# Performance work log

Hardware: AMD Instinct MI355X
Metric: run time of the kernel (lower is better)

## Reference

```python
import jax, jax.numpy as jnp
import numpy as np
import math

N, N0, M, K, CIN, COUT, DIM = 50000, 50000, 32, 15, 64, 64, 3
POINT_INFLUENCE = 0.05
KERNEL_RADIUS = 1.5 * POINT_INFLUENCE  # _INFLUENCE_TO_RADIUS * point_influence


def setup_inputs() -> dict:
    key = jax.random.key(0)
    k1, k2, k3, k4, k5, k6 = jax.random.split(key, 6)
    query_points = jax.random.uniform(k1, (N, DIM), dtype=jnp.float32)
    support_points = jax.random.uniform(k2, (N0, DIM), dtype=jnp.float32)
    # index N0 is the shadow-neighbor index (padding for ragged neighborhoods)
    neighbors = jax.random.randint(k3, (N, M), 0, N0 + 1)
    x = jax.random.normal(k4, (N0, CIN), dtype=jnp.float32)
    # kernel point dispositions inside the kernel ball, center point at origin (fixed='center')
    kp = jax.random.normal(k5, (K, DIM), dtype=jnp.float32)
    kp = kp / jnp.linalg.norm(kp, axis=1, keepdims=True) * (KERNEL_RADIUS * 0.66)
    K_points = kp.at[0].set(0.0)
    # xavier_normal_ init for weight [K, CIN, COUT]
    std = math.sqrt(2.0 / (CIN + COUT))
    weight = jax.random.normal(k6, (K, CIN, COUT), dtype=jnp.float32) * std
    return dict(query_points=query_points, support_points=support_points,
                neighbors=neighbors, x=x, K_points=K_points, weight=weight)


def reference(query_points, support_points, neighbors, x, K_points, weight):
    # shadow point far away + zero shadow feature (handles padded neighbor index N0)
    shadow_pt = jnp.full((1, support_points.shape[1]), 1e6, support_points.dtype)
    sp = jnp.concatenate([support_points, shadow_pt], axis=0)          # [N0+1, 3]
    feats = jnp.concatenate([x, jnp.zeros((1, x.shape[1]), x.dtype)], axis=0)  # [N0+1, CIN]

    # gather & center neighborhoods: [N, M, 3]
    nb_pts = sp[neighbors] - query_points[:, None, :]

    # squared distance to each kernel point without materializing [N,M,K,3]:
    # ||n - k||^2 = ||n||^2 - 2 n.k + ||k||^2  -> [N, M, K]
    sq = (jnp.sum(nb_pts * nb_pts, axis=-1)[:, :, None]
          - 2.0 * jnp.einsum('nmd,kd->nmk', nb_pts, K_points)
          + jnp.sum(K_points * K_points, axis=-1))
    sq = jnp.maximum(sq, 0.0)

    # linear KP influence: clamp(1 - dist / point_influence, min=0) -> transpose to [N, K, M]
    all_weights = jnp.maximum(1.0 - jnp.sqrt(sq) / POINT_INFLUENCE, 0.0)
    all_weights = jnp.swapaxes(all_weights, 1, 2)                      # [N, K, M]

    nb_feats = feats[neighbors]                                        # [N, M, CIN]
    weighted = jnp.matmul(all_weights, nb_feats)                       # [N, K, CIN]
    # sum over kernel points of per-kernel-point matmuls ('sum' aggregation)
    out = jnp.einsum('nkc,kco->no', weighted, weight)                  # [N, COUT]
    return out
```

## Files before the change

kernel.cpp:

```cpp
#include <hip/hip_runtime.h>

#define N_Q   50000
#define N_S   50000
#define M_NB  32
#define K_PTS 15
#define CIN   64
#define COUT  64

__global__ __launch_bounds__(256) void kpconv_fused(
    const float* __restrict__ query,
    const float* __restrict__ support,
    const int*   __restrict__ neighbors,
    const float* __restrict__ x,
    const float* __restrict__ kpts,
    const float* __restrict__ weight,
    float*       __restrict__ out)
{
    __shared__ float s_kx[K_PTS], s_ky[K_PTS], s_kz[K_PTS], s_kk[K_PTS];
    __shared__ float s_bc[4][CIN];

    const int tid = threadIdx.x;
    if (tid < K_PTS) {
        float kx = kpts[tid * 3 + 0];
        float ky = kpts[tid * 3 + 1];
        float kz = kpts[tid * 3 + 2];
        s_kx[tid] = kx; s_ky[tid] = ky; s_kz[tid] = kz;
        s_kk[tid] = kx * kx + ky * ky + kz * kz;
    }
    __syncthreads();

    const int wv   = tid >> 6;
    const int lane = tid & 63;
    const int n    = blockIdx.x * 4 + wv;

    const int m   = lane & 31;
    const int idx = neighbors[n * M_NB + m];

    float dx = 0.f, dy = 0.f, dz = 0.f, nn = 1e30f;
    if (lane < 32 && idx < N_S) {
        const float qx = query[n * 3 + 0];
        const float qy = query[n * 3 + 1];
        const float qz = query[n * 3 + 2];
        dx = support[idx * 3 + 0] - qx;
        dy = support[idx * 3 + 1] - qy;
        dz = support[idx * 3 + 2] - qz;
        nn = dx * dx + dy * dy + dz * dz;
    }

    float tout = 0.f;

    if (__ballot(nn < 0.0101f)) {
        for (int k = 0; k < K_PTS; ++k) {
            float w = 0.f;
            if (nn < 0.0101f) {
                float dot = dx * s_kx[k] + dy * s_ky[k] + dz * s_kz[k];
                float sq  = fmaxf(nn - 2.f * dot + s_kk[k], 0.f);
                if (sq < 0.0025f)
                    w = 1.f - sqrtf(sq) * 20.f;
            }
            unsigned long long em = __ballot(w > 0.f);
            if (!em) continue;

            float racc = 0.f;
            do {
                const int   src  = __ffsll(em) - 1; em &= em - 1;
                const float wsrc = __shfl(w,   src);
                const int   isrc = __shfl(idx, src);
                racc = fmaf(wsrc, x[(size_t)isrc * CIN + lane], racc);
            } while (em);

            s_bc[wv][lane] = racc;
            asm volatile("" ::: "memory");
            const float* wk = weight + (size_t)k * CIN * COUT;
            float p0 = 0.f, p1 = 0.f, p2 = 0.f, p3 = 0.f;
            #pragma unroll 8
            for (int c = 0; c < CIN; c += 4) {
                p0 = fmaf(s_bc[wv][c + 0], wk[(c + 0) * COUT + lane], p0);
                p1 = fmaf(s_bc[wv][c + 1], wk[(c + 1) * COUT + lane], p1);
                p2 = fmaf(s_bc[wv][c + 2], wk[(c + 2) * COUT + lane], p2);
                p3 = fmaf(s_bc[wv][c + 3], wk[(c + 3) * COUT + lane], p3);
            }
            tout += (p0 + p1) + (p2 + p3);
        }
    }

    out[(size_t)n * COUT + lane] = tout;
}

extern "C" void kernel_launch(void* const* d_in, const int* in_sizes, int n_in,
                              void* d_out, int out_size, void* d_ws, size_t ws_size,
                              hipStream_t stream) {
    const float* query     = (const float*)d_in[0];
    const float* support   = (const float*)d_in[1];
    const int*   neighbors = (const int*)  d_in[2];
    const float* x         = (const float*)d_in[3];
    const float* kpts      = (const float*)d_in[4];
    const float* weight    = (const float*)d_in[5];
    float*       out       = (float*)d_out;

    kpconv_fused<<<N_Q / 4, 256, 0, stream>>>(
        query, support, neighbors, x, kpts, weight, out);
}
```

Baseline: 32.52 us.

## Pack two queries per wavefront using both 32-lane halves for neighbor geometry

Each 64-lane wavefront now handles two query points, with each half computing the neighbor distances for one query, and the block shrinks to 128 threads. The kernel-point weighting and feature accumulation loop over each half's active-neighbor mask in turn. The aim is to stop leaving half the lanes idle during the geometry phase and to halve the wavefront count. In exchange, the feature gather and weight matmul are serialized per query within a wave, and the inner code is duplicated.

```diff
diff --git a/kernel.cpp b/kernel.cpp
--- a/kernel.cpp
+++ b/kernel.cpp
@@ -7,7 +7,7 @@
 #define CIN   64
 #define COUT  64
 
-__global__ __launch_bounds__(256) void kpconv_fused(
+__global__ __launch_bounds__(128) void kpconv_fused2(
     const float* __restrict__ query,
     const float* __restrict__ support,
     const int*   __restrict__ neighbors,
@@ -17,7 +17,7 @@
     float*       __restrict__ out)
 {
     __shared__ float s_kx[K_PTS], s_ky[K_PTS], s_kz[K_PTS], s_kk[K_PTS];
-    __shared__ float s_bc[4][CIN];
+    __shared__ float s_bc[2][CIN];
 
     const int tid = threadIdx.x;
     if (tid < K_PTS) {
@@ -31,23 +31,22 @@
 
     const int wv   = tid >> 6;
     const int lane = tid & 63;
-    const int n    = blockIdx.x * 4 + wv;
+    const int base = blockIdx.x * 4 + wv * 2;
+    const int h    = lane >> 5;
+    const int n    = base + h;
+    const int m    = lane & 31;
 
-    const int m   = lane & 31;
     const int idx = neighbors[n * M_NB + m];
 
     float dx = 0.f, dy = 0.f, dz = 0.f, nn = 1e30f;
-    if (lane < 32 && idx < N_S) {
-        const float qx = query[n * 3 + 0];
-        const float qy = query[n * 3 + 1];
-        const float qz = query[n * 3 + 2];
-        dx = support[idx * 3 + 0] - qx;
-        dy = support[idx * 3 + 1] - qy;
-        dz = support[idx * 3 + 2] - qz;
+    if (idx < N_S) {
+        dx = support[idx * 3 + 0] - query[n * 3 + 0];
+        dy = support[idx * 3 + 1] - query[n * 3 + 1];
+        dz = support[idx * 3 + 2] - query[n * 3 + 2];
         nn = dx * dx + dy * dy + dz * dz;
     }
 
-    float tout = 0.f;
+    float toutA = 0.f, toutB = 0.f;
 
     if (__ballot(nn < 0.0101f)) {
         for (int k = 0; k < K_PTS; ++k) {
@@ -58,33 +57,61 @@
                 if (sq < 0.0025f)
                     w = 1.f - sqrtf(sq) * 20.f;
             }
-            unsigned long long em = __ballot(w > 0.f);
+            const unsigned long long em = __ballot(w > 0.f);
             if (!em) continue;
 
-            float racc = 0.f;
-            do {
-                const int   src  = __ffsll(em) - 1; em &= em - 1;
-                const float wsrc = __shfl(w,   src);
-                const int   isrc = __shfl(idx, src);
-                racc = fmaf(wsrc, x[(size_t)isrc * CIN + lane], racc);
-            } while (em);
+            const float* wk = weight + (size_t)k * CIN * COUT;
 
-            s_bc[wv][lane] = racc;
-            asm volatile("" ::: "memory");
-            const float* wk = weight + (size_t)k * CIN * COUT;
-            float p0 = 0.f, p1 = 0.f, p2 = 0.f, p3 = 0.f;
-            #pragma unroll 8
-            for (int c = 0; c < CIN; c += 4) {
-                p0 = fmaf(s_bc[wv][c + 0], wk[(c + 0) * COUT + lane], p0);
-                p1 = fmaf(s_bc[wv][c + 1], wk[(c + 1) * COUT + lane], p1);
-                p2 = fmaf(s_bc[wv][c + 2], wk[(c + 2) * COUT + lane], p2);
-                p3 = fmaf(s_bc[wv][c + 3], wk[(c + 3) * COUT + lane], p3);
+            unsigned emA = (unsigned)(em & 0xffffffffull);
+            while (emA) {
+                float racc = 0.f;
+                do {
+                    const int src = __builtin_ctz(emA); emA &= emA - 1;
+                    const float wsrc = __shfl(w,   src);
+                    const int   isrc = __shfl(idx, src);
+                    racc = fmaf(wsrc, x[(size_t)isrc * CIN + lane], racc);
+                } while (emA);
+                s_bc[wv][lane] = racc;
+                asm volatile("" ::: "memory");
+                float p0 = 0.f, p1 = 0.f, p2 = 0.f, p3 = 0.f;
+                #pragma unroll 8
+                for (int c = 0; c < CIN; c += 4) {
+                    p0 = fmaf(s_bc[wv][c + 0], wk[(c + 0) * COUT + lane], p0);
+                    p1 = fmaf(s_bc[wv][c + 1], wk[(c + 1) * COUT + lane], p1);
+                    p2 = fmaf(s_bc[wv][c + 2], wk[(c + 2) * COUT + lane], p2);
+                    p3 = fmaf(s_bc[wv][c + 3], wk[(c + 3) * COUT + lane], p3);
+                }
+                toutA += (p0 + p1) + (p2 + p3);
+                asm volatile("" ::: "memory");
             }
-            tout += (p0 + p1) + (p2 + p3);
+
+            unsigned emB = (unsigned)(em >> 32);
+            while (emB) {
+                float racc = 0.f;
+                do {
+                    const int src = 32 + __builtin_ctz(emB); emB &= emB - 1;
+                    const float wsrc = __shfl(w,   src);
+                    const int   isrc = __shfl(idx, src);
+                    racc = fmaf(wsrc, x[(size_t)isrc * CIN + lane], racc);
+                } while (emB);
+                s_bc[wv][lane] = racc;
+                asm volatile("" ::: "memory");
+                float p0 = 0.f, p1 = 0.f, p2 = 0.f, p3 = 0.f;
+                #pragma unroll 8
+                for (int c = 0; c < CIN; c += 4) {
+                    p0 = fmaf(s_bc[wv][c + 0], wk[(c + 0) * COUT + lane], p0);
+                    p1 = fmaf(s_bc[wv][c + 1], wk[(c + 1) * COUT + lane], p1);
+                    p2 = fmaf(s_bc[wv][c + 2], wk[(c + 2) * COUT + lane], p2);
+                    p3 = fmaf(s_bc[wv][c + 3], wk[(c + 3) * COUT + lane], p3);
+                }
+                toutB += (p0 + p1) + (p2 + p3);
+                asm volatile("" ::: "memory");
+            }
         }
     }
 
-    out[(size_t)n * COUT + lane] = tout;
+    out[(size_t)(base + 0) * COUT + lane] = toutA;
+    out[(size_t)(base + 1) * COUT + lane] = toutB;
 }
 
 extern "C" void kernel_launch(void* const* d_in, const int* in_sizes, int n_in,
@@ -98,6 +125,6 @@
     const float* weight    = (const float*)d_in[5];
     float*       out       = (float*)d_out;
 
-    kpconv_fused<<<N_Q / 4, 256, 0, stream>>>(
+    kpconv_fused2<<<N_Q / 4, 128, 0, stream>>>(
         query, support, neighbors, x, kpts, weight, out);
 }
```

New measurement: 28.76 us. -11.6%, faster.

## Split into scan pass building worklist of close queries and compute pass

Applied to the files above, without the earlier changes.

Adds a scan kernel with one thread per query. It zeroes the output and tests whether any neighbor lies inside the influence threshold, then compacts the passing queries into per-wavefront worklists using a ballot and popcount. A second kernel then processes only the listed queries, and its weight matvec uses float4 loads across four channel groups with shuffle reductions. This avoids launching a wavefront for every query when most contribute nothing. The cost is an extra launch, the output zeroing traffic, and possible load imbalance across worklist segments.

```diff
diff --git a/kernel.cpp b/kernel.cpp
--- a/kernel.cpp
+++ b/kernel.cpp
@@ -6,18 +6,73 @@
 #define K_PTS 15
 #define CIN   64
 #define COUT  64
+#define THRSQ 0.0101f
+#define NWG   784
 
-__global__ __launch_bounds__(256) void kpconv_fused(
+#define WL_OFF 4096
+
+__global__ __launch_bounds__(256) void scan_kernel(
+    const float* __restrict__ query,
+    const float* __restrict__ support,
+    const int*   __restrict__ neighbors,
+    int*         __restrict__ counts,
+    int*         __restrict__ worklist,
+    float4*      __restrict__ out4)
+{
+    const int t  = blockIdx.x * 256 + threadIdx.x;
+    const int nt = gridDim.x * 256;
+
+    const float4 z = make_float4(0.f, 0.f, 0.f, 0.f);
+    for (int i = t; i < N_Q * COUT / 4; i += nt)
+        out4[i] = z;
+
+    bool close = false;
+    if (t < N_Q) {
+        const float qx = query[t * 3 + 0];
+        const float qy = query[t * 3 + 1];
+        const float qz = query[t * 3 + 2];
+        const int4* nb4 = (const int4*)(neighbors + (size_t)t * M_NB);
+        #pragma unroll
+        for (int q8 = 0; q8 < 8; ++q8) {
+            const int4 v = nb4[q8];
+            const int id[4] = { v.x, v.y, v.z, v.w };
+            #pragma unroll
+            for (int j = 0; j < 4; ++j) {
+                const int  idx   = id[j];
+                const bool valid = idx < N_S;
+                const int  ic    = valid ? idx : 0;
+                const float dx = support[ic * 3 + 0] - qx;
+                const float dy = support[ic * 3 + 1] - qy;
+                const float dz = support[ic * 3 + 2] - qz;
+                const float d2 = dx * dx + dy * dy + dz * dz;
+                close |= valid && (d2 < THRSQ);
+            }
+        }
+    }
+
+    const int lane = threadIdx.x & 63;
+    const int wgid = t >> 6;
+    const unsigned long long mask = __ballot(close);
+    if (close) {
+        const int slot = (int)__popcll(mask & ((1ull << lane) - 1ull));
+        worklist[wgid * 64 + slot] = t;
+    }
+    if (lane == 0) counts[wgid] = (int)__popcll(mask);
+}
+
+__global__ __launch_bounds__(512) void close_kernel(
     const float* __restrict__ query,
     const float* __restrict__ support,
     const int*   __restrict__ neighbors,
     const float* __restrict__ x,
     const float* __restrict__ kpts,
     const float* __restrict__ weight,
+    const int*   __restrict__ counts,
+    const int*   __restrict__ worklist,
     float*       __restrict__ out)
 {
     __shared__ float s_kx[K_PTS], s_ky[K_PTS], s_kz[K_PTS], s_kk[K_PTS];
-    __shared__ float s_bc[4][CIN];
+    __shared__ float s_bc[8][CIN];
 
     const int tid = threadIdx.x;
     if (tid < K_PTS) {
@@ -31,39 +86,42 @@
 
     const int wv   = tid >> 6;
     const int lane = tid & 63;
-    const int n    = blockIdx.x * 4 + wv;
+    const int seg  = blockIdx.x;
+    const int cnt  = counts[seg];
+    const int og   = (lane & 15) * 4;
+    const int cg   = lane >> 4;
 
-    const int m   = lane & 31;
-    const int idx = neighbors[n * M_NB + m];
+    for (int i = wv; i < cnt; i += 8) {
+        const int n = worklist[seg * 64 + i];
 
-    float dx = 0.f, dy = 0.f, dz = 0.f, nn = 1e30f;
-    if (lane < 32 && idx < N_S) {
-        const float qx = query[n * 3 + 0];
-        const float qy = query[n * 3 + 1];
-        const float qz = query[n * 3 + 2];
-        dx = support[idx * 3 + 0] - qx;
-        dy = support[idx * 3 + 1] - qy;
-        dz = support[idx * 3 + 2] - qz;
-        nn = dx * dx + dy * dy + dz * dz;
-    }
+        int idx = N_S;
+        float dx = 0.f, dy = 0.f, dz = 0.f, nn = 1e30f;
+        if (lane < 32) {
+            idx = neighbors[n * M_NB + lane];
+            if (idx < N_S) {
+                dx = support[idx * 3 + 0] - query[n * 3 + 0];
+                dy = support[idx * 3 + 1] - query[n * 3 + 1];
+                dz = support[idx * 3 + 2] - query[n * 3 + 2];
+                nn = dx * dx + dy * dy + dz * dz;
+            }
+        }
 
-    float tout = 0.f;
+        float4 tq = make_float4(0.f, 0.f, 0.f, 0.f);
 
-    if (__ballot(nn < 0.0101f)) {
         for (int k = 0; k < K_PTS; ++k) {
             float w = 0.f;
-            if (nn < 0.0101f) {
+            if (nn < THRSQ) {
                 float dot = dx * s_kx[k] + dy * s_ky[k] + dz * s_kz[k];
                 float sq  = fmaxf(nn - 2.f * dot + s_kk[k], 0.f);
                 if (sq < 0.0025f)
                     w = 1.f - sqrtf(sq) * 20.f;
             }
-            unsigned long long em = __ballot(w > 0.f);
+            unsigned em = (unsigned)__ballot(w > 0.f);
             if (!em) continue;
 
             float racc = 0.f;
             do {
-                const int   src  = __ffsll(em) - 1; em &= em - 1;
+                const int src = __builtin_ctz(em); em &= em - 1;
                 const float wsrc = __shfl(w,   src);
                 const int   isrc = __shfl(idx, src);
                 racc = fmaf(wsrc, x[(size_t)isrc * CIN + lane], racc);
@@ -71,20 +129,32 @@
 
             s_bc[wv][lane] = racc;
             asm volatile("" ::: "memory");
-            const float* wk = weight + (size_t)k * CIN * COUT;
-            float p0 = 0.f, p1 = 0.f, p2 = 0.f, p3 = 0.f;
-            #pragma unroll 8
-            for (int c = 0; c < CIN; c += 4) {
-                p0 = fmaf(s_bc[wv][c + 0], wk[(c + 0) * COUT + lane], p0);
-                p1 = fmaf(s_bc[wv][c + 1], wk[(c + 1) * COUT + lane], p1);
-                p2 = fmaf(s_bc[wv][c + 2], wk[(c + 2) * COUT + lane], p2);
-                p3 = fmaf(s_bc[wv][c + 3], wk[(c + 3) * COUT + lane], p3);
+            const float* wq = weight + (size_t)k * CIN * COUT + cg * COUT + og;
+            float4 a0 = make_float4(0.f,0.f,0.f,0.f);
+            float4 a1 = make_float4(0.f,0.f,0.f,0.f);
+            #pragma unroll
+            for (int q = 0; q < 16; q += 2) {
+                const float4 v0 = *(const float4*)(wq + (q + 0) * 4 * COUT);
+                const float4 v1 = *(const float4*)(wq + (q + 1) * 4 * COUT);
+                const float xc0 = s_bc[wv][cg + 4 * q];
+                const float xc1 = s_bc[wv][cg + 4 * q + 4];
+                a0.x = fmaf(xc0, v0.x, a0.x); a0.y = fmaf(xc0, v0.y, a0.y);
+                a0.z = fmaf(xc0, v0.z, a0.z); a0.w = fmaf(xc0, v0.w, a0.w);
+                a1.x = fmaf(xc1, v1.x, a1.x); a1.y = fmaf(xc1, v1.y, a1.y);
+                a1.z = fmaf(xc1, v1.z, a1.z); a1.w = fmaf(xc1, v1.w, a1.w);
             }
-            tout += (p0 + p1) + (p2 + p3);
+            a0.x += a1.x; a0.y += a1.y; a0.z += a1.z; a0.w += a1.w;
+            a0.x += __shfl_xor(a0.x, 16); a0.y += __shfl_xor(a0.y, 16);
+            a0.z += __shfl_xor(a0.z, 16); a0.w += __shfl_xor(a0.w, 16);
+            a0.x += __shfl_xor(a0.x, 32); a0.y += __shfl_xor(a0.y, 32);
+            a0.z += __shfl_xor(a0.z, 32); a0.w += __shfl_xor(a0.w, 32);
+            tq.x += a0.x; tq.y += a0.y; tq.z += a0.z; tq.w += a0.w;
+            asm volatile("" ::: "memory");
         }
+
+        float4* row = (float4*)(out + (size_t)n * COUT);
+        if (lane < 16) row[lane] = tq;
     }
-
-    out[(size_t)n * COUT + lane] = tout;
 }
 
 extern "C" void kernel_launch(void* const* d_in, const int* in_sizes, int n_in,
@@ -98,6 +168,11 @@
     const float* weight    = (const float*)d_in[5];
     float*       out       = (float*)d_out;
 
-    kpconv_fused<<<N_Q / 4, 256, 0, stream>>>(
-        query, support, neighbors, x, kpts, weight, out);
+    int* counts   = (int*)d_ws;
+    int* worklist = (int*)((char*)d_ws + WL_OFF);
+
+    scan_kernel<<<196, 256, 0, stream>>>(
+        query, support, neighbors, counts, worklist, (float4*)out);
+    close_kernel<<<NWG, 512, 0, stream>>>(
+        query, support, neighbors, x, kpts, weight, counts, worklist, out);
 }
```

New measurement: 36.74 us. +13.0%, slower.

## Process four queries per wavefront with full-lane neighbor mapping and float4 weight tiles

Applied to the files above, without the earlier changes.

Each 64-lane wavefront now handles four query points instead of one: every lane owns one neighbor of two query pairs, so all lanes do useful distance work where half sat idle before. The per-kernel-point weight matvec is restructured so each lane computes four output channels over a quarter of the input channels, reading float4 weight vectors, then reduces across lane groups with xor shuffles. Block size drops to 128 threads covering 8 queries. The aim is better lane utilization and fewer, wider weight loads, at the cost of more shuffles, more registers and more serialized event branches per wavefront.

```diff
diff --git a/kernel.cpp b/kernel.cpp
--- a/kernel.cpp
+++ b/kernel.cpp
@@ -6,8 +6,45 @@
 #define K_PTS 15
 #define CIN   64
 #define COUT  64
+#define THR   0.0101f
 
-__global__ __launch_bounds__(256) void kpconv_fused(
+__device__ __forceinline__ void do_event(
+    unsigned em, int laneoff, float w, int idx,
+    float* bc, const float* wq, int cg,
+    const float* __restrict__ x, int lane, float4& tout)
+{
+    float racc = 0.f;
+    do {
+        const int src = laneoff + __builtin_ctz(em); em &= em - 1;
+        const float wsrc = __shfl(w,   src);
+        const int   isrc = __shfl(idx, src);
+        racc = fmaf(wsrc, x[(size_t)isrc * CIN + lane], racc);
+    } while (em);
+    bc[lane] = racc;
+    asm volatile("" ::: "memory");
+    float4 a0 = make_float4(0.f, 0.f, 0.f, 0.f);
+    float4 a1 = make_float4(0.f, 0.f, 0.f, 0.f);
+    #pragma unroll
+    for (int i = 0; i < 16; i += 2) {
+        const float4 v0 = *(const float4*)(wq + (i + 0) * 4 * COUT);
+        const float4 v1 = *(const float4*)(wq + (i + 1) * 4 * COUT);
+        const float xc0 = bc[cg + 4 * i];
+        const float xc1 = bc[cg + 4 * i + 4];
+        a0.x = fmaf(xc0, v0.x, a0.x); a0.y = fmaf(xc0, v0.y, a0.y);
+        a0.z = fmaf(xc0, v0.z, a0.z); a0.w = fmaf(xc0, v0.w, a0.w);
+        a1.x = fmaf(xc1, v1.x, a1.x); a1.y = fmaf(xc1, v1.y, a1.y);
+        a1.z = fmaf(xc1, v1.z, a1.z); a1.w = fmaf(xc1, v1.w, a1.w);
+    }
+    a0.x += a1.x; a0.y += a1.y; a0.z += a1.z; a0.w += a1.w;
+    a0.x += __shfl_xor(a0.x, 16); a0.y += __shfl_xor(a0.y, 16);
+    a0.z += __shfl_xor(a0.z, 16); a0.w += __shfl_xor(a0.w, 16);
+    a0.x += __shfl_xor(a0.x, 32); a0.y += __shfl_xor(a0.y, 32);
+    a0.z += __shfl_xor(a0.z, 32); a0.w += __shfl_xor(a0.w, 32);
+    tout.x += a0.x; tout.y += a0.y; tout.z += a0.z; tout.w += a0.w;
+    asm volatile("" ::: "memory");
+}
+
+__global__ __launch_bounds__(128) void kpconv_fused6(
     const float* __restrict__ query,
     const float* __restrict__ support,
     const int*   __restrict__ neighbors,
@@ -17,7 +54,7 @@
     float*       __restrict__ out)
 {
     __shared__ float s_kx[K_PTS], s_ky[K_PTS], s_kz[K_PTS], s_kk[K_PTS];
-    __shared__ float s_bc[4][CIN];
+    __shared__ float s_bc[2][CIN];
 
     const int tid = threadIdx.x;
     if (tid < K_PTS) {
@@ -31,60 +68,71 @@
 
     const int wv   = tid >> 6;
     const int lane = tid & 63;
-    const int n    = blockIdx.x * 4 + wv;
+    const int base = blockIdx.x * 8 + wv * 4;
+    const int h    = lane >> 5;
 
-    const int m   = lane & 31;
-    const int idx = neighbors[n * M_NB + m];
+    const int idx0 = neighbors[(size_t)(base + 0) * M_NB + lane];
+    const int idx1 = neighbors[(size_t)(base + 2) * M_NB + lane];
 
-    float dx = 0.f, dy = 0.f, dz = 0.f, nn = 1e30f;
-    if (lane < 32 && idx < N_S) {
-        const float qx = query[n * 3 + 0];
-        const float qy = query[n * 3 + 1];
-        const float qz = query[n * 3 + 2];
-        dx = support[idx * 3 + 0] - qx;
-        dy = support[idx * 3 + 1] - qy;
-        dz = support[idx * 3 + 2] - qz;
-        nn = dx * dx + dy * dy + dz * dz;
-    }
+    const bool val0 = idx0 < N_S;
+    const bool val1 = idx1 < N_S;
+    const int  ic0  = val0 ? idx0 : 0;
+    const int  ic1  = val1 ? idx1 : 0;
+    const float sx0 = support[ic0 * 3 + 0], sy0 = support[ic0 * 3 + 1], sz0 = support[ic0 * 3 + 2];
+    const float sx1 = support[ic1 * 3 + 0], sy1 = support[ic1 * 3 + 1], sz1 = support[ic1 * 3 + 2];
 
-    float tout = 0.f;
+    const int n0 = base + h, n1 = base + 2 + h;
+    const float dx0 = sx0 - query[n0 * 3 + 0];
+    const float dy0 = sy0 - query[n0 * 3 + 1];
+    const float dz0 = sz0 - query[n0 * 3 + 2];
+    const float dx1 = sx1 - query[n1 * 3 + 0];
+    const float dy1 = sy1 - query[n1 * 3 + 1];
+    const float dz1 = sz1 - query[n1 * 3 + 2];
+    float nn0 = dx0 * dx0 + dy0 * dy0 + dz0 * dz0;
+    float nn1 = dx1 * dx1 + dy1 * dy1 + dz1 * dz1;
+    if (!val0) nn0 = 1e30f;
+    if (!val1) nn1 = 1e30f;
 
-    if (__ballot(nn < 0.0101f)) {
+    const int og = (lane & 15) * 4;
+    const int cg = lane >> 4;
+
+    float4 t0 = make_float4(0.f,0.f,0.f,0.f), t1 = make_float4(0.f,0.f,0.f,0.f);
+    float4 t2 = make_float4(0.f,0.f,0.f,0.f), t3 = make_float4(0.f,0.f,0.f,0.f);
+
+    if (__ballot(fminf(nn0, nn1) < THR)) {
+        #pragma unroll 1
         for (int k = 0; k < K_PTS; ++k) {
-            float w = 0.f;
-            if (nn < 0.0101f) {
-                float dot = dx * s_kx[k] + dy * s_ky[k] + dz * s_kz[k];
-                float sq  = fmaxf(nn - 2.f * dot + s_kk[k], 0.f);
-                if (sq < 0.0025f)
-                    w = 1.f - sqrtf(sq) * 20.f;
+            float w0 = 0.f, w1 = 0.f;
+            if (nn0 < THR) {
+                float dot = dx0 * s_kx[k] + dy0 * s_ky[k] + dz0 * s_kz[k];
+                float sq  = fmaxf(nn0 - 2.f * dot + s_kk[k], 0.f);
+                if (sq < 0.0025f) w0 = 1.f - sqrtf(sq) * 20.f;
             }
-            unsigned long long em = __ballot(w > 0.f);
-            if (!em) continue;
+            if (nn1 < THR) {
+                float dot = dx1 * s_kx[k] + dy1 * s_ky[k] + dz1 * s_kz[k];
+                float sq  = fmaxf(nn1 - 2.f * dot + s_kk[k], 0.f);
+                if (sq < 0.0025f) w1 = 1.f - sqrtf(sq) * 20.f;
+            }
+            const unsigned long long em0 = __ballot(w0 > 0.f);
+            const unsigned long long em1 = __ballot(w1 > 0.f);
+            if (!(em0 | em1)) continue;
 
-            float racc = 0.f;
-            do {
-                const int   src  = __ffsll(em) - 1; em &= em - 1;
-                const float wsrc = __shfl(w,   src);
-                const int   isrc = __shfl(idx, src);
-                racc = fmaf(wsrc, x[(size_t)isrc * CIN + lane], racc);
-            } while (em);
-
-            s_bc[wv][lane] = racc;
-            asm volatile("" ::: "memory");
-            const float* wk = weight + (size_t)k * CIN * COUT;
-            float p0 = 0.f, p1 = 0.f, p2 = 0.f, p3 = 0.f;
-            #pragma unroll 8
-            for (int c = 0; c < CIN; c += 4) {
-                p0 = fmaf(s_bc[wv][c + 0], wk[(c + 0) * COUT + lane], p0);
-                p1 = fmaf(s_bc[wv][c + 1], wk[(c + 1) * COUT + lane], p1);
-                p2 = fmaf(s_bc[wv][c + 2], wk[(c + 2) * COUT + lane], p2);
-                p3 = fmaf(s_bc[wv][c + 3], wk[(c + 3) * COUT + lane], p3);
-            }
-            tout += (p0 + p1) + (p2 + p3);
+            const float* wq = weight + (size_t)k * CIN * COUT + cg * COUT + og;
+            unsigned m;
+            if ((m = (unsigned)(em0 & 0xffffffffull)))
+                do_event(m,  0, w0, idx0, s_bc[wv], wq, cg, x, lane, t0);
+            if ((m = (unsigned)(em0 >> 32)))
+                do_event(m, 32, w0, idx0, s_bc[wv], wq, cg, x, lane, t1);
+            if ((m = (unsigned)(em1 & 0xffffffffull)))
+                do_event(m,  0, w1, idx1, s_bc[wv], wq, cg, x, lane, t2);
+            if ((m = (unsigned)(em1 >> 32)))
+                do_event(m, 32, w1, idx1, s_bc[wv], wq, cg, x, lane, t3);
         }
     }
 
-    out[(size_t)n * COUT + lane] = tout;
+    const float4 tsel = (lane < 16) ? t0 : (lane < 32) ? t1
+                      : (lane < 48) ? t2 : t3;
+    ((float4*)out)[(size_t)base * (COUT / 4) + lane] = tsel;
 }
 
 extern "C" void kernel_launch(void* const* d_in, const int* in_sizes, int n_in,
@@ -98,6 +146,6 @@
     const float* weight    = (const float*)d_in[5];
     float*       out       = (float*)d_out;
 
-    kpconv_fused<<<N_Q / 4, 256, 0, stream>>>(
+    kpconv_fused6<<<N_Q / 8, 128, 0, stream>>>(
         query, support, neighbors, x, kpts, weight, out);
 }
```

Result: faster. 28.68 us (-11.8%).
